# Performance work log

Measured on AMD Instinct MI355X. Metric: run time of the kernel, lower is better.

## Reference

```python
import jax, jax.numpy as jnp
import numpy as np

# Loihi neuron constants (from init params: iDecay=1024, vDecay=128, vThMant=80, wgtExp=0)
I_DECAY = 1024.0
V_DECAY = 128.0
THETA = 80.0 * 64.0       # vThMant << 6
W_SCALE = 64.0            # 1 << (6 + wgtExp)


def _trunc_decay(s, decay):
    # Loihi fixed-point decay: trunc(s * (4096 - decay) / 4096)
    smooth = s * ((4096.0 - decay) / 4096.0)
    return smooth + jax.lax.stop_gradient(jnp.trunc(smooth) - smooth)


def _loihi(x):
    # x: [N, C, T] weighted spikes -> binary spikes [N, C, T]
    zero = jnp.zeros(x.shape[:-1], x.dtype)

    def step(carry, xt):
        u, v = carry
        u = _trunc_decay(u, I_DECAY) + W_SCALE * xt
        v = _trunc_decay(v, V_DECAY) + u
        spike = (v >= THETA).astype(v.dtype)
        v = v * (1.0 - spike)  # reset on spike (refDelay=1)
        return (u, v), spike

    _, s = jax.lax.scan(step, (zero, zero), jnp.moveaxis(x, -1, 0))
    return jnp.moveaxis(s, 0, -1)


def _delay_shift(x):
    # shift spike train by one time step along last axis
    return jnp.pad(x, ((0, 0), (0, 0), (1, 0)))[..., :-1]


def setup_inputs() -> dict:
    key = jax.random.key(0)
    k = jax.random.split(key, 5)
    N, T = 32, 400
    spike_rate = 0.1
    tact = (jax.random.uniform(k[0], (N, 156, T)) < spike_rate).astype(jnp.float32)
    vis = (jax.random.uniform(k[1], (N, 6300, T)) < spike_rate).astype(jnp.float32)
    W_tact = 0.1 * jax.random.normal(k[2], (512, 156), jnp.float32)
    W_vis = 0.1 * jax.random.normal(k[3], (512, 6300), jnp.float32)
    W_combi = 0.1 * jax.random.normal(k[4], (256, 1024), jnp.float32)
    return {"spikeInputTact": tact, "spikeInputVis": vis,
            "W_tact": W_tact, "W_vis": W_vis, "W_combi": W_combi}


def reference(spikeInputTact, spikeInputVis, W_tact, W_vis, W_combi):
    # dense = per-time-step linear: [o,i] x [n,i,t] -> [n,o,t]
    tact = _delay_shift(_loihi(jnp.einsum('oi,nit->not', W_tact, spikeInputTact)))
    vis = _delay_shift(_loihi(jnp.einsum('oi,nit->not', W_vis, spikeInputVis)))
    combi = jnp.concatenate([tact, vis], axis=1)  # [N, 1024, T]
    out = _delay_shift(_loihi(jnp.einsum('oi,nit->not', W_combi, combi)))
    return out
```

## Files before the change

kernel.cpp:

```cpp
#include <hip/hip_runtime.h>


typedef unsigned short u16;
typedef unsigned int u32;
typedef __attribute__((ext_vector_type(8))) short short8;
typedef __attribute__((ext_vector_type(4))) float f32x4;

#define GLOAD16(g, l)                                                         \
    __builtin_amdgcn_global_load_lds(                                         \
        (const __attribute__((address_space(1))) u32*)(g),                    \
        (__attribute__((address_space(3))) u32*)(l), 16, 0, 0)

__device__ __forceinline__ u16 f2bf_trunc(float x) {
    return (u16)(__float_as_uint(x) >> 16);
}

__device__ __forceinline__ void cvt_body(const float* __restrict__ S,
                                         u16* __restrict__ Sp,
                                         int I, int KLD, int n, int i0, int t0,
                                         u16 (*tile)[88])
{
    const int tid = threadIdx.x;
    const int il = tid >> 2;
    const int q  = tid & 3;
    const int gi = i0 + il;
    const bool iok = gi < I;
    const float* srow = S + ((size_t)n * I + gi) * 400 + t0;

    #pragma unroll
    for (int s = 0; s < 4; ++s) {
        const int fi = s * 4 + q;
        const int tl = fi * 4;
        float4 v = make_float4(0.f, 0.f, 0.f, 0.f);
        if (iok && (t0 + tl) < 400)
            v = *(const float4*)(srow + tl);
        tile[tl + 0][il] = f2bf_trunc(v.x);
        tile[tl + 1][il] = f2bf_trunc(v.y);
        tile[tl + 2][il] = f2bf_trunc(v.z);
        tile[tl + 3][il] = f2bf_trunc(v.w);
    }
    __syncthreads();

    const int tl = tid >> 2;
    const int iq = tid & 3;
    const int t  = t0 + tl;
    const int go = i0 + iq * 16;
    if (t < 400 && go < KLD) {
        u16* dst = Sp + (size_t)(n * 400 + t) * KLD + go;
        *(short8*)(dst)     = *(const short8*)&tile[tl][iq * 16];
        *(short8*)(dst + 8) = *(const short8*)&tile[tl][iq * 16 + 8];
    }
}

__device__ __forceinline__ void split_one(const float* __restrict__ W,
                                          u16* __restrict__ W2,
                                          int C, int K, int KLD, int idx)
{
    const int c = idx / KLD;
    const int k = idx - c * KLD;
    float w = (k < K) ? W[(size_t)c * K + k] : 0.f;
    u32 b  = __float_as_uint(w);
    u32 hb = (b + 0x7FFFu + ((b >> 16) & 1u)) & 0xFFFF0000u;
    float r = w - __uint_as_float(hb);
    u32 rb = __float_as_uint(r);
    u32 mb = (rb + 0x7FFFu + ((rb >> 16) & 1u)) & 0xFFFF0000u;
    const int rh = ((c >> 4) << 5) | (c & 15);
    W2[(size_t)rh * KLD + k]        = (u16)(hb >> 16);
    W2[(size_t)(rh + 16) * KLD + k] = (u16)(mb >> 16);
}

__global__ __launch_bounds__(256) void prep(
    const float* __restrict__ vis, const float* __restrict__ tact,
    const float* __restrict__ Wv, const float* __restrict__ Wt,
    const float* __restrict__ Wc,
    u16* __restrict__ Sv, u16* __restrict__ St,
    u16* __restrict__ Wv2, u16* __restrict__ Wt2, u16* __restrict__ Wc2)
{
    __shared__ u16 tile[64][88];
    const int b = blockIdx.x;
    if (b < 22400) {
        const int x = b % 7, y = (b / 7) % 100, n = b / 700;
        cvt_body(vis, Sv, 6300, 6400, n, y * 64, x * 64, tile);
    } else if (b < 23296) {
        const int b2 = b - 22400;
        const int x = b2 % 7, y = (b2 / 7) % 4, n = b2 / 28;
        cvt_body(tact, St, 156, 256, n, y * 64, x * 64, tile);
    } else {
        const int b3 = b - 23296;
        for (int e = b3 * 256 + (int)threadIdx.x; e < 3670016; e += 1024 * 256) {
            if (e < 3276800)        split_one(Wv, Wv2, 512, 6300, 6400, e);
            else if (e < 3407872)   split_one(Wt, Wt2, 512, 156,  256,  e - 3276800);
            else                    split_one(Wc, Wc2, 256, 1024, 1024, e - 3407872);
        }
    }
}

__device__ __forceinline__ void gemm_core(
    const u16* __restrict__ A, const u16* __restrict__ B,
    float* __restrict__ X, int M2, int KLD, int kt0, int nk,
    int bx, int by, u16* lds)
{
    const int c0  = bx * 256;
    const int nt0 = by * 256;
    const int tid  = threadIdx.x;
    const int lane = tid & 63, w = tid >> 6;
    const int wm = w >> 2, wn = w & 3;
    const int l15 = lane & 15, l16 = lane >> 4;

    const int swzg  = (l16 ^ ((l15 >> 1) & 3)) * 8;
    const int aBase = (wm * 128 + l15) * 32 + swzg;
    const int bBase = 16384 + (wn * 64 + l15) * 32 + swzg;

    const int gsw = ((tid & 3) ^ ((tid >> 3) & 3)) * 8;
    const u16* pA = A + (size_t)(c0 + (tid >> 2)) * KLD + gsw;
    const u16* pB = B + (size_t)(nt0 + (tid >> 2)) * KLD + gsw;
    u16* const ldsW = &lds[w * 512];

#define STG(op, d, ks, tt) do {                                               \
    const u16* s_ = ((op) ? pB : pA) + (size_t)(tt) * 64 + (ks) * 32;         \
    GLOAD16(s_, ldsW + (d) * 32768 + (op) * 16384 + (ks) * 8192);             \
    GLOAD16(s_ + (size_t)128 * KLD,                                           \
            ldsW + (d) * 32768 + (op) * 16384 + (ks) * 8192 + 4096);          \
} while (0)

#define PH(d, ks, mh, LOADB, STAGE_STMT, WAIT_STMT) do {                      \
    short8 a_[4];                                                             \
    _Pragma("unroll")                                                         \
    for (int mf = 0; mf < 4; ++mf)                                            \
        a_[mf] = *(const short8*)&lds[(d) * 32768 + (ks) * 8192 + aBase       \
                                      + ((mh) * 4 + mf) * 512];               \
    if (LOADB) {                                                              \
        _Pragma("unroll")                                                     \
        for (int nf = 0; nf < 4; ++nf)                                        \
            bcur[nf] = *(const short8*)&lds[(d) * 32768 + (ks) * 8192 + bBase \
                                            + nf * 512];                      \
    }                                                                         \
    STAGE_STMT;                                                               \
    __builtin_amdgcn_s_barrier();                                             \
    asm volatile("s_waitcnt lgkmcnt(0)" ::: "memory");                        \
    __builtin_amdgcn_sched_barrier(0);                                        \
    __builtin_amdgcn_s_setprio(1);                                            \
    _Pragma("unroll")                                                         \
    for (int mf = 0; mf < 4; ++mf)                                            \
        _Pragma("unroll")                                                     \
        for (int nf = 0; nf < 4; ++nf)                                        \
            acc[(mh) * 4 + mf][nf] = __builtin_amdgcn_mfma_f32_16x16x32_bf16( \
                a_[mf], bcur[nf], acc[(mh) * 4 + mf][nf], 0, 0, 0);           \
    __builtin_amdgcn_s_setprio(0);                                            \
    WAIT_STMT;                                                                \
    __builtin_amdgcn_s_barrier();                                             \
    asm volatile("" ::: "memory");                                            \
} while (0)

    f32x4 acc[8][4];
    #pragma unroll
    for (int i = 0; i < 8; ++i)
        #pragma unroll
        for (int j = 0; j < 4; ++j)
            acc[i][j] = (f32x4){0.f, 0.f, 0.f, 0.f};

    STG(0, 0, 0, kt0); STG(1, 0, 0, kt0); STG(0, 0, 1, kt0); STG(1, 0, 1, kt0);
    STG(0, 1, 0, kt0 + 1); STG(1, 1, 0, kt0 + 1); STG(1, 1, 1, kt0 + 1);
    asm volatile("s_waitcnt vmcnt(0)" ::: "memory");
    __builtin_amdgcn_s_barrier();
    asm volatile("" ::: "memory");

    const int I = nk >> 1;
    for (int i = 0; i < I; ++i) {
        const int t = kt0 + 2 * i;
        const bool pf = (i < I - 1);
        short8 bcur[4];
        PH(0, 0, 0, 1, { STG(0, 1, 1, t + 1); }, );
        PH(0, 0, 1, 0, { if (pf) STG(1, 0, 0, t + 2); }, );
        PH(0, 1, 0, 1, { if (pf) STG(0, 0, 0, t + 2); }, );
        PH(0, 1, 1, 0, { if (pf) STG(1, 0, 1, t + 2); },
           { if (pf) asm volatile("s_waitcnt vmcnt(6)" ::: "memory");
             else    asm volatile("s_waitcnt vmcnt(0)" ::: "memory"); });
        PH(1, 0, 0, 1, { if (pf) STG(0, 0, 1, t + 2); }, );
        PH(1, 0, 1, 0, { if (pf) STG(1, 1, 0, t + 3); }, );
        PH(1, 1, 0, 1, { if (pf) STG(0, 1, 0, t + 3); }, );
        PH(1, 1, 1, 0, { if (pf) STG(1, 1, 1, t + 3); },
           { if (pf) asm volatile("s_waitcnt vmcnt(6)" ::: "memory");
             else    asm volatile("s_waitcnt vmcnt(0)" ::: "memory"); });
    }

    const int Mout = M2 >> 1;
    #pragma unroll
    for (int j = 0; j < 4; ++j) {
        const int cg = bx * 128 + wm * 64 + j * 16 + l16 * 4;
        #pragma unroll
        for (int nf = 0; nf < 4; ++nf) {
            const int nt = nt0 + wn * 64 + nf * 16 + l15;
            f32x4 s = acc[2 * j][nf] + acc[2 * j + 1][nf];
            *(f32x4*)&X[(size_t)nt * Mout + cg] = s;
        }
    }
#undef STG
#undef PH
}

__global__ __launch_bounds__(512, 2) void gemm_l1(
    const u16* __restrict__ Av, const u16* __restrict__ Bv, float* __restrict__ Xv,
    const u16* __restrict__ At, const u16* __restrict__ Bt, float* __restrict__ Xt)
{
    __shared__ u16 lds[65536];
    const int f = blockIdx.x + 4 * (blockIdx.y + 50 * blockIdx.z);
    if (f < 400) {
        const int p   = (f & 7) >> 1;
        const int k   = ((f >> 3) << 1) | (f & 1);
        const int bx  = k & 3;
        const int pi  = 25 * p + (k >> 2);
        const int by  = pi % 50;
        const int bz  = pi / 50;
        gemm_core(Av, Bv, Xv + (size_t)bz * 12800 * 512, 1024, 6400,
                  bz * 50, 50, bx, by, lds);
    } else {
        const int f2 = f - 400;
        gemm_core(At, Bt, Xt, 1024, 256, 0, 4, f2 & 3, f2 >> 2, lds);
    }
}

__global__ __launch_bounds__(512, 2) void gemm_g(
    const u16* __restrict__ A, const u16* __restrict__ B,
    float* __restrict__ Xbase, int M2, int KLD, int ktPerZ)
{
    __shared__ u16 lds[65536];
    const int Dx = gridDim.x, Dy = gridDim.y;
    int f = blockIdx.x + Dx * (blockIdx.y + Dy * blockIdx.z);
    const int nwg = Dx * Dy * gridDim.z;
    f = (f & 7) * (nwg >> 3) + (f >> 3);
    const int bx = f % Dx;
    const int by = (f / Dx) % Dy;
    const int bz = f / (Dx * Dy);
    gemm_core(A, B, Xbase + (size_t)bz * 12800 * (M2 >> 1), M2, KLD,
              bz * ktPerZ, ktPerZ, bx, by, lds);
}

__device__ __forceinline__ float loihi_step(float xt, float& u, float& v)
{
    u = truncf(u * 0.75f) + 64.f * xt;
    v = truncf(v * 0.96875f) + u;
    if (v >= 5120.f) { v = 0.f; return 1.f; }
    return 0.f;
}

__global__ __launch_bounds__(64) void scan_ab(const float* __restrict__ Xt,
                                              const float* __restrict__ Xv,
                                              u16* __restrict__ Sc)
{
    const int gid = blockIdx.x * 64 + threadIdx.x;
    const int n = gid >> 10;
    const int c = gid & 1023;
    const size_t PS = (size_t)12800 * 512;
    const bool isv = (c >= 512);
    const float* xr = isv ? (Xv + (size_t)(n * 400) * 512 + (c - 512))
                          : (Xt + (size_t)(n * 400) * 512 + c);
    u16* srow = Sc + (size_t)(n * 400) * 1024 + c;
    srow[0] = 0;

    float a0[8], b0[8], a1[8], b1[8], a2[8], b2[8];
    #pragma unroll
    for (int d = 0; d < 8; ++d) {
        a0[d] = xr[(size_t)d * 512];
        b0[d] = isv ? xr[(size_t)d * 512 + PS] : 0.f;
    }
    #pragma unroll
    for (int d = 0; d < 8; ++d) {
        a1[d] = xr[(size_t)(8 + d) * 512];
        b1[d] = isv ? xr[(size_t)(8 + d) * 512 + PS] : 0.f;
    }

    float u = 0.f, v = 0.f;
    for (int blk = 0; blk < 50; ++blk) {
        const int tb = blk * 8;
        #pragma unroll
        for (int d = 0; d < 8; ++d) {
            const int tl = tb + 16 + d;
            a2[d] = (tl < 400) ? xr[(size_t)tl * 512] : 0.f;
            b2[d] = (isv && tl < 400) ? xr[(size_t)tl * 512 + PS] : 0.f;
        }
        #pragma unroll
        for (int d = 0; d < 8; ++d) {
            const int t = tb + d;
            const float sp = loihi_step(a0[d] + b0[d], u, v);
            if (t < 399) srow[(size_t)(t + 1) * 1024] = (sp != 0.f) ? (u16)0x3F80 : (u16)0;
        }
        #pragma unroll
        for (int d = 0; d < 8; ++d) {
            a0[d] = a1[d]; b0[d] = b1[d];
            a1[d] = a2[d]; b1[d] = b2[d];
        }
    }
}

__global__ __launch_bounds__(64) void scan_c(const float* __restrict__ Xc,
                                             float* __restrict__ out)
{
    const int gid = blockIdx.x * 64 + threadIdx.x;
    const int n = gid >> 8;
    const int c = gid & 255;
    const size_t PS = (size_t)12800 * 256;
    const float* xr = Xc + (size_t)(n * 400) * 256 + c;
    float* orow = out + ((size_t)n * 256 + c) * 400;
    orow[0] = 0.f;

    float a0[8], b0[8], a1[8], b1[8], a2[8], b2[8];
    #pragma unroll
    for (int d = 0; d < 8; ++d) {
        a0[d] = xr[(size_t)d * 256];
        b0[d] = xr[(size_t)d * 256 + PS];
    }
    #pragma unroll
    for (int d = 0; d < 8; ++d) {
        a1[d] = xr[(size_t)(8 + d) * 256];
        b1[d] = xr[(size_t)(8 + d) * 256 + PS];
    }

    float u = 0.f, v = 0.f;
    for (int blk = 0; blk < 50; ++blk) {
        const int tb = blk * 8;
        #pragma unroll
        for (int d = 0; d < 8; ++d) {
            const int tl = tb + 16 + d;
            a2[d] = (tl < 400) ? xr[(size_t)tl * 256] : 0.f;
            b2[d] = (tl < 400) ? xr[(size_t)tl * 256 + PS] : 0.f;
        }
        #pragma unroll
        for (int d = 0; d < 8; ++d) {
            const int t = tb + d;
            const float sp = loihi_step(a0[d] + b0[d], u, v);
            if (t < 399) orow[t + 1] = sp;
        }
        #pragma unroll
        for (int d = 0; d < 8; ++d) {
            a0[d] = a1[d]; b0[d] = b1[d];
            a1[d] = a2[d]; b1[d] = b2[d];
        }
    }
}

extern "C" void kernel_launch(void* const* d_in, const int* in_sizes, int n_in,
                              void* d_out, int out_size, void* d_ws, size_t ws_size,
                              hipStream_t stream)
{
    const float* tact   = (const float*)d_in[0];
    const float* vis    = (const float*)d_in[1];
    const float* W_tact = (const float*)d_in[2];
    const float* W_vis  = (const float*)d_in[3];
    const float* W_comb = (const float*)d_in[4];
    float* out = (float*)d_out;

    const int NT = 32 * 400;
    const int Ktp = 256;
    const int Kvp = 6400;
    const int Kc  = 1024;

    char* p = (char*)d_ws;
    u16* Sv  = (u16*)p;                p += (size_t)NT * Kvp * 2;
    u16* St  = (u16*)p;                p += (size_t)NT * Ktp * 2;
    u16* Wt2 = (u16*)p;                p += (size_t)1024 * Ktp * 2;
    u16* Wv2 = (u16*)p;                p += (size_t)1024 * Kvp * 2;
    u16* Wc2 = (u16*)p;                p += (size_t)512 * Kc * 2;
    float* Xv = (float*)p;             p += (size_t)2 * NT * 512 * 4;
    float* Xt = (float*)p;             p += (size_t)NT * 512 * 4;
    u16*   Sc = (u16*)Sv;
    float* Xc = (float*)((char*)Sv + (size_t)NT * 1024 * 2);

    prep<<<dim3(24320), 256, 0, stream>>>(vis, tact, W_vis, W_tact, W_comb,
                                          Sv, St, Wv2, Wt2, Wc2);

    gemm_l1<<<dim3(4, 50, 3), 512, 0, stream>>>(Wv2, Sv, Xv, Wt2, St, Xt);

    scan_ab<<<dim3((32 * 1024) / 64), 64, 0, stream>>>(Xt, Xv, Sc);

    gemm_g<<<dim3(2, 50, 2), 512, 0, stream>>>(Wc2, Sc, Xc, 512, Kc, 8);
    scan_c<<<dim3((32 * 256) / 64), 64, 0, stream>>>(Xc, out);

    (void)in_sizes; (void)n_in; (void)out_size; (void)ws_size;
}
```

Baseline: 366.3 us.

## Drop split-K for vision GEMM and widen input conversion tiles

```diff
diff --git a/kernel.cpp b/kernel.cpp
--- a/kernel.cpp
+++ b/kernel.cpp
@@ -3,6 +3,7 @@
 
 typedef unsigned short u16;
 typedef unsigned int u32;
+typedef __attribute__((ext_vector_type(4))) short short4v;
 typedef __attribute__((ext_vector_type(8))) short short8;
 typedef __attribute__((ext_vector_type(4))) float f32x4;
 
@@ -13,6 +14,53 @@
 
 __device__ __forceinline__ u16 f2bf_trunc(float x) {
     return (u16)(__float_as_uint(x) >> 16);
+}
+
+__device__ __forceinline__ void cvt_wide(const float* __restrict__ S,
+                                         u16* __restrict__ Sp,
+                                         int I, int KLD, int n, int i0, int t0,
+                                         u16 (*tile)[268])
+{
+    const int tid = threadIdx.x;
+    const int il = tid >> 2;
+    const int q  = tid & 3;
+
+    #pragma unroll
+    for (int ii = 0; ii < 4; ++ii) {
+        const int gi = i0 + ii * 64 + il;
+        const bool iok = gi < I;
+        const float* srow = S + ((size_t)n * I + gi) * 400 + t0;
+        #pragma unroll
+        for (int s = 0; s < 4; ++s) {
+            const int tl = (s * 4 + q) * 4;
+            float4 v = make_float4(0.f, 0.f, 0.f, 0.f);
+            if (iok && (t0 + tl) < 400)
+                v = *(const float4*)(srow + tl);
+            tile[tl + 0][ii * 64 + il] = f2bf_trunc(v.x);
+            tile[tl + 1][ii * 64 + il] = f2bf_trunc(v.y);
+            tile[tl + 2][ii * 64 + il] = f2bf_trunc(v.z);
+            tile[tl + 3][ii * 64 + il] = f2bf_trunc(v.w);
+        }
+    }
+    __syncthreads();
+
+    const int row = tid >> 3;
+    const int lc  = tid & 7;
+    #pragma unroll
+    for (int h = 0; h < 2; ++h) {
+        const int tl = h * 32 + row;
+        const int t = t0 + tl;
+        if (t < 400) {
+            u16* dst = Sp + (size_t)(n * 400 + t) * KLD + i0;
+            #pragma unroll
+            for (int w = 0; w < 4; ++w) {
+                const int io = w * 64 + lc * 8;
+                *(short4v*)(dst + io)     = *(const short4v*)&tile[tl][io];
+                *(short4v*)(dst + io + 4) = *(const short4v*)&tile[tl][io + 4];
+            }
+        }
+    }
+    __syncthreads();
 }
 
 __device__ __forceinline__ void cvt_body(const float* __restrict__ S,
@@ -29,8 +77,7 @@
 
     #pragma unroll
     for (int s = 0; s < 4; ++s) {
-        const int fi = s * 4 + q;
-        const int tl = fi * 4;
+        const int tl = (s * 4 + q) * 4;
         float4 v = make_float4(0.f, 0.f, 0.f, 0.f);
         if (iok && (t0 + tl) < 400)
             v = *(const float4*)(srow + tl);
@@ -50,6 +97,7 @@
         *(short8*)(dst)     = *(const short8*)&tile[tl][iq * 16];
         *(short8*)(dst + 8) = *(const short8*)&tile[tl][iq * 16 + 8];
     }
+    __syncthreads();
 }
 
 __device__ __forceinline__ void split_one(const float* __restrict__ W,
@@ -76,17 +124,17 @@
     u16* __restrict__ Sv, u16* __restrict__ St,
     u16* __restrict__ Wv2, u16* __restrict__ Wt2, u16* __restrict__ Wc2)
 {
-    __shared__ u16 tile[64][88];
+    __shared__ u16 tile[64][268];
     const int b = blockIdx.x;
-    if (b < 22400) {
-        const int x = b % 7, y = (b / 7) % 100, n = b / 700;
-        cvt_body(vis, Sv, 6300, 6400, n, y * 64, x * 64, tile);
-    } else if (b < 23296) {
-        const int b2 = b - 22400;
+    if (b < 5600) {
+        const int x = b % 7, y = (b / 7) % 25, n = b / 175;
+        cvt_wide(vis, Sv, 6300, 6400, n, y * 256, x * 64, tile);
+    } else if (b < 6496) {
+        const int b2 = b - 5600;
         const int x = b2 % 7, y = (b2 / 7) % 4, n = b2 / 28;
-        cvt_body(tact, St, 156, 256, n, y * 64, x * 64, tile);
+        cvt_body(tact, St, 156, 256, n, y * 64, x * 64, (u16(*)[88])tile);
     } else {
-        const int b3 = b - 23296;
+        const int b3 = b - 6496;
         for (int e = b3 * 256 + (int)threadIdx.x; e < 3670016; e += 1024 * 256) {
             if (e < 3276800)        split_one(Wv, Wv2, 512, 6300, 6400, e);
             else if (e < 3407872)   split_one(Wt, Wt2, 512, 156,  256,  e - 3276800);
@@ -205,17 +253,20 @@
 {
     __shared__ u16 lds[65536];
     const int f = blockIdx.x + 4 * (blockIdx.y + 50 * blockIdx.z);
-    if (f < 400) {
-        const int p   = (f & 7) >> 1;
-        const int k   = ((f >> 3) << 1) | (f & 1);
-        const int bx  = k & 3;
-        const int pi  = 25 * p + (k >> 2);
-        const int by  = pi % 50;
-        const int bz  = pi / 50;
-        gemm_core(Av, Bv, Xv + (size_t)bz * 12800 * 512, 1024, 6400,
-                  bz * 50, 50, bx, by, lds);
+    if (f < 200) {
+        int bx, by;
+        if (f < 192) {
+            const int m = f >> 4, r = f & 15;
+            by = m * 4 + ((r & 7) >> 1);
+            bx = ((r >> 3) << 1) | (r & 1);
+        } else {
+            const int k = f - 192;
+            by = 48 + (k >> 2);
+            bx = k & 3;
+        }
+        gemm_core(Av, Bv, Xv, 1024, 6400, 0, 100, bx, by, lds);
     } else {
-        const int f2 = f - 400;
+        const int f2 = f - 200;
         gemm_core(At, Bt, Xt, 1024, 256, 0, 4, f2 & 3, f2 >> 2, lds);
     }
 }
@@ -251,24 +302,17 @@
     const int gid = blockIdx.x * 64 + threadIdx.x;
     const int n = gid >> 10;
     const int c = gid & 1023;
-    const size_t PS = (size_t)12800 * 512;
-    const bool isv = (c >= 512);
-    const float* xr = isv ? (Xv + (size_t)(n * 400) * 512 + (c - 512))
-                          : (Xt + (size_t)(n * 400) * 512 + c);
+    const float* xr = (c < 512)
+        ? Xt + (size_t)(n * 400) * 512 + c
+        : Xv + (size_t)(n * 400) * 512 + (c - 512);
     u16* srow = Sc + (size_t)(n * 400) * 1024 + c;
     srow[0] = 0;
 
-    float a0[8], b0[8], a1[8], b1[8], a2[8], b2[8];
-    #pragma unroll
-    for (int d = 0; d < 8; ++d) {
-        a0[d] = xr[(size_t)d * 512];
-        b0[d] = isv ? xr[(size_t)d * 512 + PS] : 0.f;
-    }
-    #pragma unroll
-    for (int d = 0; d < 8; ++d) {
-        a1[d] = xr[(size_t)(8 + d) * 512];
-        b1[d] = isv ? xr[(size_t)(8 + d) * 512 + PS] : 0.f;
-    }
+    float c0[8], c1[8], c2[8];
+    #pragma unroll
+    for (int d = 0; d < 8; ++d) c0[d] = xr[(size_t)d * 512];
+    #pragma unroll
+    for (int d = 0; d < 8; ++d) c1[d] = xr[(size_t)(8 + d) * 512];
 
     float u = 0.f, v = 0.f;
     for (int blk = 0; blk < 50; ++blk) {
@@ -276,20 +320,16 @@
         #pragma unroll
         for (int d = 0; d < 8; ++d) {
             const int tl = tb + 16 + d;
-            a2[d] = (tl < 400) ? xr[(size_t)tl * 512] : 0.f;
-            b2[d] = (isv && tl < 400) ? xr[(size_t)tl * 512 + PS] : 0.f;
+            c2[d] = (tl < 400) ? xr[(size_t)tl * 512] : 0.f;
         }
         #pragma unroll
         for (int d = 0; d < 8; ++d) {
             const int t = tb + d;
-            const float sp = loihi_step(a0[d] + b0[d], u, v);
+            const float sp = loihi_step(c0[d], u, v);
             if (t < 399) srow[(size_t)(t + 1) * 1024] = (sp != 0.f) ? (u16)0x3F80 : (u16)0;
         }
         #pragma unroll
-        for (int d = 0; d < 8; ++d) {
-            a0[d] = a1[d]; b0[d] = b1[d];
-            a1[d] = a2[d]; b1[d] = b2[d];
-        }
+        for (int d = 0; d < 8; ++d) { c0[d] = c1[d]; c1[d] = c2[d]; }
     }
 }
 
@@ -361,15 +401,15 @@
     u16* Wt2 = (u16*)p;                p += (size_t)1024 * Ktp * 2;
     u16* Wv2 = (u16*)p;                p += (size_t)1024 * Kvp * 2;
     u16* Wc2 = (u16*)p;                p += (size_t)512 * Kc * 2;
-    float* Xv = (float*)p;             p += (size_t)2 * NT * 512 * 4;
+    float* Xv = (float*)p;             p += (size_t)NT * 512 * 4;
     float* Xt = (float*)p;             p += (size_t)NT * 512 * 4;
     u16*   Sc = (u16*)Sv;
     float* Xc = (float*)((char*)Sv + (size_t)NT * 1024 * 2);
 
-    prep<<<dim3(24320), 256, 0, stream>>>(vis, tact, W_vis, W_tact, W_comb,
-                                          Sv, St, Wv2, Wt2, Wc2);
-
-    gemm_l1<<<dim3(4, 50, 3), 512, 0, stream>>>(Wv2, Sv, Xv, Wt2, St, Xt);
+    prep<<<dim3(7520), 256, 0, stream>>>(vis, tact, W_vis, W_tact, W_comb,
+                                         Sv, St, Wv2, Wt2, Wc2);
+
+    gemm_l1<<<dim3(4, 50, 2), 512, 0, stream>>>(Wv2, Sv, Xv, Wt2, St, Xt);
 
     scan_ab<<<dim3((32 * 1024) / 64), 64, 0, stream>>>(Xt, Xv, Sc);
 
```

New measurement: 354.9 us. 3.1% less time.
